# Performance work log

Measured on AMD Instinct MI355X. Metric: run time of the kernel, lower is better.

The kernel has to match this reference:

```python
import jax, jax.numpy as jnp
import numpy as np

B = 2048   # number of samples; acts as seq_len for the (S,N,E) transformer
DIN = 768
D = 512    # hidden_dim
H = 8      # nheads
HD = D // H
L = 3      # encoder layers
P = 40     # num_prototypes
Q = D // 4 # 128, projected feature dim
EPS = 1e-5


def setup_inputs() -> dict:
    key = jax.random.key(0)
    ks = jax.random.split(key, 22)
    s = 0.02
    rn = lambda k, shape: jax.random.normal(k, shape, jnp.float32) * s
    return {
        "x": jax.random.normal(ks[0], (B, DIN), jnp.float32),
        "reduce_w": rn(ks[1], (D, DIN)), "reduce_b": rn(ks[2], (D,)),
        "in_w": rn(ks[3], (L, 3 * D, D)), "in_b": rn(ks[4], (L, 3 * D)),
        "out_w": rn(ks[5], (L, D, D)), "out_b": rn(ks[6], (L, D)),
        "ff1_w": rn(ks[7], (L, D, D)), "ff1_b": rn(ks[8], (L, D)),
        "ff2_w": rn(ks[9], (L, D, D)), "ff2_b": rn(ks[10], (L, D)),
        "ln1_w": jnp.ones((L, D), jnp.float32), "ln1_b": jnp.zeros((L, D), jnp.float32),
        "ln2_w": jnp.ones((L, D), jnp.float32), "ln2_b": jnp.zeros((L, D), jnp.float32),
        "mlp_w1": rn(ks[11], (D, D)), "mlp_b1": rn(ks[12], (D,)),
        "mlp_w2": rn(ks[13], (D, D)), "mlp_b2": rn(ks[14], (D,)),
        "mlp_w3": rn(ks[15], (Q, D)), "mlp_b3": rn(ks[16], (Q,)),
        "highlights": jax.random.normal(ks[17], (P, Q), jnp.float32),
        "negatives": jax.random.normal(ks[18], (P, Q), jnp.float32),
    }


def _inorm(x):
    # InstanceNorm1d (affine=False) on a 2D tensor: per-row normalize over last dim
    m = x.mean(-1, keepdims=True)
    v = ((x - m) ** 2).mean(-1, keepdims=True)  # biased variance, matches torch
    return (x - m) * jax.lax.rsqrt(v + EPS)


def _ln(x, w, b):
    m = x.mean(-1, keepdims=True)
    v = ((x - m) ** 2).mean(-1, keepdims=True)
    return (x - m) * jax.lax.rsqrt(v + EPS) * w + b


def _cdist(a, cb):
    # euclidean distances [B,P]
    d2 = (a * a).sum(-1, keepdims=True) + (cb * cb).sum(-1) - 2.0 * a @ cb.T
    return jnp.sqrt(jnp.maximum(d2, 0.0))


def reference(x, reduce_w, reduce_b, in_w, in_b, out_w, out_b,
              ff1_w, ff1_b, ff2_w, ff2_b, ln1_w, ln1_b, ln2_w, ln2_b,
              mlp_w1, mlp_b1, mlp_w2, mlp_b2, mlp_w3, mlp_b3,
              highlights, negatives):
    feat0 = _inorm(x @ reduce_w.T + reduce_b)  # [B,D]

    # TransformerEncoder, post-norm, relu FFN, dropout off (eval).
    # Input is (seq=B, batch=1, D) -> attention across all B rows.
    feat = feat0
    scale = 1.0 / np.sqrt(HD)
    for i in range(L):
        qkv = feat @ in_w[i].T + in_b[i]           # [B,3D]
        q, k, v = jnp.split(qkv, 3, axis=-1)
        q = q.reshape(B, H, HD)
        k = k.reshape(B, H, HD)
        v = v.reshape(B, H, HD)
        scores = jnp.einsum('ihd,jhd->hij', q, k) * scale  # [H,B,B]
        attn = jax.nn.softmax(scores, axis=-1)
        ctx = jnp.einsum('hij,jhd->ihd', attn, v).reshape(B, D)
        attn_out = ctx @ out_w[i].T + out_b[i]
        feat = _ln(feat + attn_out, ln1_w[i], ln1_b[i])
        ff = jax.nn.relu(feat @ ff1_w[i].T + ff1_b[i]) @ ff2_w[i].T + ff2_b[i]
        feat = _ln(feat + ff, ln2_w[i], ln2_b[i])

    feat = feat0 + _inorm(feat)

    # MLP 512 -> 512 -> 512 -> 128 (relu on all but last)
    feat = jax.nn.relu(feat @ mlp_w1.T + mlp_b1)
    feat = jax.nn.relu(feat @ mlp_w2.T + mlp_b2)
    feat = feat @ mlp_w3.T + mlp_b3
    feat = _inorm(feat)  # [B,Q]

    positive_dist = _cdist(feat, highlights).min(-1)
    negative_dist = _cdist(feat, negatives).min(-1)
    logits = jnp.stack([-negative_dist, -positive_dist], axis=-1)  # [B,2]
    return logits
```

## Files before the change

kernel.cpp:

```cpp
#include <hip/hip_runtime.h>
#include <math.h>
#include <cstddef>

#define EPS 1e-5f

typedef __attribute__((ext_vector_type(8))) short bf16x8;
typedef __attribute__((ext_vector_type(4))) float f32x4;

__device__ __forceinline__ float wave_sum(float v) {
#pragma unroll
  for (int o = 32; o > 0; o >>= 1) v += __shfl_xor(v, o, 64);
  return v;
}

__device__ __forceinline__ unsigned short f2b(float f) {
  union { float f; unsigned int u; } v; v.f = f;
  unsigned int r = (v.u + 0x7FFFu + ((v.u >> 16) & 1u)) >> 16;
  return (unsigned short)r;
}
__device__ __forceinline__ float b2f(unsigned short u) {
  union { unsigned int u; float f; } v; v.u = ((unsigned int)u) << 16;
  return v.f;
}

__device__ __forceinline__ unsigned int pk2(float lo, float hi) {
  unsigned int r;
  asm volatile("v_cvt_pk_bf16_f32 %0, %1, %2" : "=v"(r) : "v"(lo), "v"(hi));
  return r;
}

struct WConvArgs {
  const float* src[8];
  unsigned short* dst[8];
  int n[8];
};
__global__ __launch_bounds__(256) void conv_w(WConvArgs a) {
  const int arr = blockIdx.y;
  const int i = (blockIdx.x * 256 + threadIdx.x) * 4;
  if (i >= a.n[arr]) return;
  const float4 f = *(const float4*)(a.src[arr] + i);
  unsigned short t[4] = {f2b(f.x), f2b(f.y), f2b(f.z), f2b(f.w)};
  unsigned short* d = a.dst[arr] + i;
  *(ushort2*)d = *(ushort2*)&t[0];
  *(ushort2*)(d + 2) = *(ushort2*)&t[2];
}

template <int RELU, int AF32, int OUT_F32, int OUT_BF16, int MERGE, int RESID,
          int SCALEQ>
__global__ __launch_bounds__(256) void gemm32(
    const void* __restrict__ Aptr, const float* __restrict__ pmp,
    const unsigned short* __restrict__ W, const float* __restrict__ bias,
    const float* __restrict__ Rf, float* __restrict__ Cf,
    unsigned short* __restrict__ Cb, int M, int N, int K) {
  __shared__ __align__(16) unsigned short As[2][32][72];
  __shared__ __align__(16) unsigned short Ws[2][64][72];
  const int tid = threadIdx.x;
  const int wid = tid >> 6, lane = tid & 63;
  const int ln = lane & 15, quad = lane >> 4;
  const int m0 = blockIdx.x * 32, n0 = blockIdx.y * 64;
  const int arow = tid >> 3, aseg = tid & 7;
  const int wrow = tid >> 2, wseg = tid & 3;
  const int KS = K >> 6;

  bf16x8 ra;
  float4 ra32[2];
  bf16x8 rwb0, rwb1;
  bf16x8 rp[4];
  float rl;

  auto load_tile = [&](int ks) {
    const int k0 = ks * 64;
    if (MERGE) {
      const int h = ks;
      const int row = m0 + arow;
      rl = 0.f;
#pragma unroll
      for (int s = 0; s < 4; ++s) {
        const size_t b = (size_t)((s * 8 + h) * 2048 + row);
        rl += pmp[b];
        rp[s] = *(const bf16x8*)((const unsigned short*)Aptr + b * 64 + aseg * 8);
      }
    } else if (AF32) {
      const float* ap = (const float*)Aptr + (size_t)(m0 + arow) * K + k0 + aseg * 8;
      ra32[0] = *(const float4*)ap;
      ra32[1] = *(const float4*)(ap + 4);
    } else {
      ra = *(const bf16x8*)((const unsigned short*)Aptr +
                            (size_t)(m0 + arow) * K + k0 + aseg * 8);
    }
    const unsigned short* wp = W + (size_t)(n0 + wrow) * K + k0 + wseg * 16;
    rwb0 = *(const bf16x8*)wp;
    rwb1 = *(const bf16x8*)(wp + 8);
  };

  auto store_tile = [&](int buf) {
    if (MERGE) {
      float inv = 1.f / rl;
      unsigned short ta[8];
#pragma unroll
      for (int j = 0; j < 8; ++j) {
        float s = b2f((unsigned short)rp[0][j]) + b2f((unsigned short)rp[1][j]) +
                  b2f((unsigned short)rp[2][j]) + b2f((unsigned short)rp[3][j]);
        ta[j] = f2b(inv * s);
      }
      *(bf16x8*)&As[buf][arow][aseg * 8] = *(const bf16x8*)&ta[0];
    } else if (AF32) {
      unsigned short ta[8];
      ta[0] = f2b(ra32[0].x); ta[1] = f2b(ra32[0].y);
      ta[2] = f2b(ra32[0].z); ta[3] = f2b(ra32[0].w);
      ta[4] = f2b(ra32[1].x); ta[5] = f2b(ra32[1].y);
      ta[6] = f2b(ra32[1].z); ta[7] = f2b(ra32[1].w);
      *(bf16x8*)&As[buf][arow][aseg * 8] = *(const bf16x8*)&ta[0];
    } else {
      *(bf16x8*)&As[buf][arow][aseg * 8] = ra;
    }
    *(bf16x8*)&Ws[buf][wrow][wseg * 16] = rwb0;
    *(bf16x8*)&Ws[buf][wrow][wseg * 16 + 8] = rwb1;
  };

  f32x4 acc[2];
  acc[0] = (f32x4){0.f, 0.f, 0.f, 0.f};
  acc[1] = (f32x4){0.f, 0.f, 0.f, 0.f};

  const int mrow = (wid & 1) * 16, nh = wid >> 1;

  load_tile(0);
  store_tile(0);
  __syncthreads();

#pragma unroll 1
  for (int ks = 0; ks < KS; ++ks) {
    const int cur = ks & 1;
    if (ks + 1 < KS) load_tile(ks + 1);
#pragma unroll
    for (int kc = 0; kc < 2; ++kc) {
      bf16x8 af = *(const bf16x8*)&As[cur][mrow + ln][kc * 32 + quad * 8];
#pragma unroll
      for (int nt = 0; nt < 2; ++nt) {
        bf16x8 wf = *(const bf16x8*)&Ws[cur][nh * 32 + nt * 16 + ln][kc * 32 + quad * 8];
        acc[nt] = __builtin_amdgcn_mfma_f32_16x16x32_bf16(af, wf, acc[nt], 0, 0, 0);
      }
    }
    if (ks + 1 < KS) store_tile(cur ^ 1);
    __syncthreads();
  }

  const int gm = m0 + mrow + quad * 4;
  const float qs = (SCALEQ && n0 < 512) ? 0.125f : 1.f;
#pragma unroll
  for (int nt = 0; nt < 2; ++nt) {
    const int gn = n0 + nh * 32 + nt * 16 + ln;
    float bv = bias[gn];
#pragma unroll
    for (int r = 0; r < 4; ++r) {
      float v = acc[nt][r] + bv;
      if (SCALEQ) v *= qs;
      if (RELU) v = fmaxf(v, 0.f);
      if (RESID) v += Rf[(size_t)(gm + r) * N + gn];
      if (OUT_F32) Cf[(size_t)(gm + r) * N + gn] = v;
      if (OUT_BF16) Cb[(size_t)(gm + r) * N + gn] = f2b(v);
    }
  }
}

__global__ __launch_bounds__(256) void flash_attn8(
    const unsigned short* __restrict__ qkv, float* __restrict__ pm,
    unsigned short* __restrict__ po) {
  __shared__ __align__(16) unsigned short Ks[64][72];
  __shared__ __align__(16) unsigned short Vt[64][72];
  __shared__ __align__(16) unsigned int Pp[64][36];
  const int qt = blockIdx.x, h = blockIdx.y, sp = blockIdx.z;
  const int tid = threadIdx.x;
  const int wid = tid >> 6, lane = tid & 63;
  const int ln = lane & 15, quad = lane >> 4;
  const int wq0 = wid * 16;

  bf16x8 aq[2];
  {
    const unsigned short* qp =
        qkv + (size_t)(qt * 64 + wq0 + ln) * 1536 + h * 64 + quad * 8;
    aq[0] = *(const bf16x8*)qp;
    aq[1] = *(const bf16x8*)(qp + 32);
  }

  const int key = tid >> 2, seg = tid & 3;
  bf16x8 rk0, rk1;
  unsigned short tv[16];

  auto load_kv = [&](int t) {
    const int g = sp * 8 + t;
    const unsigned short* kr =
        qkv + (size_t)(g * 64 + key) * 1536 + 512 + h * 64 + seg * 16;
    rk0 = *(const bf16x8*)kr;
    rk1 = *(const bf16x8*)(kr + 8);
#pragma unroll
    for (int j = 0; j < 16; ++j)
      tv[j] = qkv[(size_t)(g * 64 + wid * 16 + j) * 1536 + 1024 + h * 64 + lane];
  };
  auto store_kv = [&]() {
    *(bf16x8*)&Ks[key][seg * 16] = rk0;
    *(bf16x8*)&Ks[key][seg * 16 + 8] = rk1;
    *(bf16x8*)&Vt[lane][wid * 16] = *(const bf16x8*)&tv[0];
    *(bf16x8*)&Vt[lane][wid * 16 + 8] = *(const bf16x8*)&tv[8];
  };

  float l_r = 0.f;
  f32x4 acc_o[4];
#pragma unroll
  for (int nt = 0; nt < 4; ++nt) acc_o[nt] = (f32x4){0.f, 0.f, 0.f, 0.f};

  load_kv(0);
  store_kv();
  __syncthreads();

#pragma unroll 1
  for (int t = 0; t < 8; ++t) {
    if (t + 1 < 8) load_kv(t + 1);

    f32x4 s_acc[4];
#pragma unroll
    for (int nt = 0; nt < 4; ++nt) s_acc[nt] = (f32x4){0.f, 0.f, 0.f, 0.f};
#pragma unroll
    for (int nt = 0; nt < 4; ++nt) {
      bf16x8 kf0 = *(const bf16x8*)&Ks[nt * 16 + ln][quad * 8];
      bf16x8 kf1 = *(const bf16x8*)&Ks[nt * 16 + ln][32 + quad * 8];
      s_acc[nt] = __builtin_amdgcn_mfma_f32_16x16x32_bf16(kf0, aq[0], s_acc[nt], 0, 0, 0);
      s_acc[nt] = __builtin_amdgcn_mfma_f32_16x16x32_bf16(kf1, aq[1], s_acc[nt], 0, 0, 0);
    }

#pragma unroll
    for (int nt = 0; nt < 4; ++nt) {
      float p0 = __expf(s_acc[nt][0]);
      float p1 = __expf(s_acc[nt][1]);
      float p2 = __expf(s_acc[nt][2]);
      float p3 = __expf(s_acc[nt][3]);
      l_r += (p0 + p1) + (p2 + p3);
      uint2 w;
      w.x = pk2(p0, p1);
      w.y = pk2(p2, p3);
      *(uint2*)&Pp[wq0 + ln][nt * 8 + quad * 2] = w;
    }

#pragma unroll
    for (int kc = 0; kc < 2; ++kc) {
      bf16x8 pf = *(const bf16x8*)&Pp[wq0 + ln][kc * 16 + quad * 4];
#pragma unroll
      for (int nt = 0; nt < 4; ++nt) {
        bf16x8 vf = *(const bf16x8*)&Vt[nt * 16 + ln][kc * 32 + quad * 8];
        acc_o[nt] = __builtin_amdgcn_mfma_f32_16x16x32_bf16(pf, vf, acc_o[nt], 0, 0, 0);
      }
    }
    __syncthreads();
    if (t + 1 < 8) {
      store_kv();
      __syncthreads();
    }
  }

  const size_t base = (size_t)((sp * 8 + h) * 2048 + qt * 64);
  float l = l_r;
  l += __shfl_xor(l, 16, 64);
  l += __shfl_xor(l, 32, 64);
  if (quad == 0) pm[base + wq0 + ln] = l;
#pragma unroll
  for (int r = 0; r < 4; ++r) {
    const size_t row = base + wq0 + quad * 4 + r;
#pragma unroll
    for (int nt = 0; nt < 4; ++nt)
      po[row * 64 + nt * 16 + ln] = f2b(acc_o[nt][r]);
  }
}

__global__ __launch_bounds__(256) void inorm512(float* __restrict__ dst,
                                                unsigned short* __restrict__ dstb,
                                                const float* __restrict__ src) {
  const int row = blockIdx.x * 4 + (threadIdx.x >> 6);
  const int lane = threadIdx.x & 63;
  const float4* s = (const float4*)(src + (size_t)row * 512);
  float4 a = s[lane], b = s[lane + 64];
  float sum = a.x + a.y + a.z + a.w + b.x + b.y + b.z + b.w;
  float mean = wave_sum(sum) * (1.f / 512.f);
  float vs = (a.x - mean) * (a.x - mean) + (a.y - mean) * (a.y - mean) +
             (a.z - mean) * (a.z - mean) + (a.w - mean) * (a.w - mean) +
             (b.x - mean) * (b.x - mean) + (b.y - mean) * (b.y - mean) +
             (b.z - mean) * (b.z - mean) + (b.w - mean) * (b.w - mean);
  float rs = rsqrtf(wave_sum(vs) * (1.f / 512.f) + EPS);
  float4 oa, obv;
  oa.x = (a.x - mean) * rs; oa.y = (a.y - mean) * rs;
  oa.z = (a.z - mean) * rs; oa.w = (a.w - mean) * rs;
  obv.x = (b.x - mean) * rs; obv.y = (b.y - mean) * rs;
  obv.z = (b.z - mean) * rs; obv.w = (b.w - mean) * rs;
  float4* d = (float4*)(dst + (size_t)row * 512);
  d[lane] = oa; d[lane + 64] = obv;
  unsigned short* db = dstb + (size_t)row * 512;
  unsigned short t0[4] = {f2b(oa.x), f2b(oa.y), f2b(oa.z), f2b(oa.w)};
  unsigned short t1[4] = {f2b(obv.x), f2b(obv.y), f2b(obv.z), f2b(obv.w)};
  *(ushort2*)&db[lane * 4] = *(ushort2*)&t0[0];
  *(ushort2*)&db[lane * 4 + 2] = *(ushort2*)&t0[2];
  *(ushort2*)&db[256 + lane * 4] = *(ushort2*)&t1[0];
  *(ushort2*)&db[256 + lane * 4 + 2] = *(ushort2*)&t1[2];
}

__global__ __launch_bounds__(256) void ln_res2(float* __restrict__ dst,
                                               unsigned short* __restrict__ dstb,
                                               const float* __restrict__ src,
                                               const float* __restrict__ w,
                                               const float* __restrict__ bb) {
  const int row = blockIdx.x * 4 + (threadIdx.x >> 6);
  const int lane = threadIdx.x & 63;
  const float4* xs = (const float4*)(src + (size_t)row * 512);
  float4 a = xs[lane], b = xs[lane + 64];
  float sum = a.x + a.y + a.z + a.w + b.x + b.y + b.z + b.w;
  float mean = wave_sum(sum) * (1.f / 512.f);
  float vs = (a.x - mean) * (a.x - mean) + (a.y - mean) * (a.y - mean) +
             (a.z - mean) * (a.z - mean) + (a.w - mean) * (a.w - mean) +
             (b.x - mean) * (b.x - mean) + (b.y - mean) * (b.y - mean) +
             (b.z - mean) * (b.z - mean) + (b.w - mean) * (b.w - mean);
  float rs = rsqrtf(wave_sum(vs) * (1.f / 512.f) + EPS);
  float4 wa = ((const float4*)w)[lane], wb = ((const float4*)w)[lane + 64];
  float4 ba = ((const float4*)bb)[lane], bbv = ((const float4*)bb)[lane + 64];
  float4 oa, ob2;
  oa.x = (a.x - mean) * rs * wa.x + ba.x; oa.y = (a.y - mean) * rs * wa.y + ba.y;
  oa.z = (a.z - mean) * rs * wa.z + ba.z; oa.w = (a.w - mean) * rs * wa.w + ba.w;
  ob2.x = (b.x - mean) * rs * wb.x + bbv.x; ob2.y = (b.y - mean) * rs * wb.y + bbv.y;
  ob2.z = (b.z - mean) * rs * wb.z + bbv.z; ob2.w = (b.w - mean) * rs * wb.w + bbv.w;
  float4* d = (float4*)(dst + (size_t)row * 512);
  d[lane] = oa; d[lane + 64] = ob2;
  unsigned short* dbp = dstb + (size_t)row * 512;
  unsigned short t0[4] = {f2b(oa.x), f2b(oa.y), f2b(oa.z), f2b(oa.w)};
  unsigned short t1[4] = {f2b(ob2.x), f2b(ob2.y), f2b(ob2.z), f2b(ob2.w)};
  *(ushort2*)&dbp[lane * 4] = *(ushort2*)&t0[0];
  *(ushort2*)&dbp[lane * 4 + 2] = *(ushort2*)&t0[2];
  *(ushort2*)&dbp[256 + lane * 4] = *(ushort2*)&t1[0];
  *(ushort2*)&dbp[256 + lane * 4 + 2] = *(ushort2*)&t1[2];
}

__global__ __launch_bounds__(256) void add_inorm(float* __restrict__ feat,
                                                 unsigned short* __restrict__ featb,
                                                 const float* __restrict__ feat0) {
  const int row = blockIdx.x * 4 + (threadIdx.x >> 6);
  const int lane = threadIdx.x & 63;
  float4* f = (float4*)(feat + (size_t)row * 512);
  const float4* f0 = (const float4*)(feat0 + (size_t)row * 512);
  float4 a = f[lane], b = f[lane + 64];
  float sum = a.x + a.y + a.z + a.w + b.x + b.y + b.z + b.w;
  float mean = wave_sum(sum) * (1.f / 512.f);
  float vs = (a.x - mean) * (a.x - mean) + (a.y - mean) * (a.y - mean) +
             (a.z - mean) * (a.z - mean) + (a.w - mean) * (a.w - mean) +
             (b.x - mean) * (b.x - mean) + (b.y - mean) * (b.y - mean) +
             (b.z - mean) * (b.z - mean) + (b.w - mean) * (b.w - mean);
  float rs = rsqrtf(wave_sum(vs) * (1.f / 512.f) + EPS);
  float4 za = f0[lane], zb = f0[lane + 64];
  float4 oa, ob2;
  oa.x = za.x + (a.x - mean) * rs; oa.y = za.y + (a.y - mean) * rs;
  oa.z = za.z + (a.z - mean) * rs; oa.w = za.w + (a.w - mean) * rs;
  ob2.x = zb.x + (b.x - mean) * rs; ob2.y = zb.y + (b.y - mean) * rs;
  ob2.z = zb.z + (b.z - mean) * rs; ob2.w = zb.w + (b.w - mean) * rs;
  f[lane] = oa; f[lane + 64] = ob2;
  unsigned short* dbp = featb + (size_t)row * 512;
  unsigned short t0[4] = {f2b(oa.x), f2b(oa.y), f2b(oa.z), f2b(oa.w)};
  unsigned short t1[4] = {f2b(ob2.x), f2b(ob2.y), f2b(ob2.z), f2b(ob2.w)};
  *(ushort2*)&dbp[lane * 4] = *(ushort2*)&t0[0];
  *(ushort2*)&dbp[lane * 4 + 2] = *(ushort2*)&t0[2];
  *(ushort2*)&dbp[256 + lane * 4] = *(ushort2*)&t1[0];
  *(ushort2*)&dbp[256 + lane * 4 + 2] = *(ushort2*)&t1[2];
}

__global__ __launch_bounds__(256) void dist2(const float* __restrict__ fq,
                                             const float* __restrict__ hi,
                                             const float* __restrict__ ne,
                                             float* __restrict__ out) {
  const int row = blockIdx.x * 4 + (threadIdx.x >> 6);
  const int lane = threadIdx.x & 63;
  float f0 = fq[(size_t)row * 128 + lane];
  float f1 = fq[(size_t)row * 128 + 64 + lane];
  float mean = wave_sum(f0 + f1) * (1.f / 128.f);
  float vs = (f0 - mean) * (f0 - mean) + (f1 - mean) * (f1 - mean);
  float rs = rsqrtf(wave_sum(vs) * (1.f / 128.f) + EPS);
  f0 = (f0 - mean) * rs;
  f1 = (f1 - mean) * rs;
  float mp = 1e30f, mn = 1e30f;
  for (int p = 0; p < 40; ++p) {
    float h0 = hi[p * 128 + lane], h1 = hi[p * 128 + 64 + lane];
    float d0 = f0 - h0, d1 = f1 - h1;
    float d2 = wave_sum(d0 * d0 + d1 * d1);
    mp = fminf(mp, d2);
    float n0 = ne[p * 128 + lane], n1 = ne[p * 128 + 64 + lane];
    d0 = f0 - n0; d1 = f1 - n1;
    d2 = wave_sum(d0 * d0 + d1 * d1);
    mn = fminf(mn, d2);
  }
  if (lane == 0) {
    out[row * 2 + 0] = -sqrtf(mn);
    out[row * 2 + 1] = -sqrtf(mp);
  }
}

extern "C" void kernel_launch(void* const* d_in, const int* in_sizes, int n_in,
                              void* d_out, int out_size, void* d_ws, size_t ws_size,
                              hipStream_t stream) {
  const float* x        = (const float*)d_in[0];
  const float* reduce_w = (const float*)d_in[1];
  const float* reduce_b = (const float*)d_in[2];
  const float* in_w     = (const float*)d_in[3];
  const float* in_b     = (const float*)d_in[4];
  const float* out_w    = (const float*)d_in[5];
  const float* out_b    = (const float*)d_in[6];
  const float* ff1_w    = (const float*)d_in[7];
  const float* ff1_b    = (const float*)d_in[8];
  const float* ff2_w    = (const float*)d_in[9];
  const float* ff2_b    = (const float*)d_in[10];
  const float* ln1_w    = (const float*)d_in[11];
  const float* ln1_b    = (const float*)d_in[12];
  const float* ln2_w    = (const float*)d_in[13];
  const float* ln2_b    = (const float*)d_in[14];
  const float* mlp_w1   = (const float*)d_in[15];
  const float* mlp_b1   = (const float*)d_in[16];
  const float* mlp_w2   = (const float*)d_in[17];
  const float* mlp_b2   = (const float*)d_in[18];
  const float* mlp_w3   = (const float*)d_in[19];
  const float* mlp_b3   = (const float*)d_in[20];
  const float* hi       = (const float*)d_in[21];
  const float* ne       = (const float*)d_in[22];
  float* out = (float*)d_out;
  float* ws = (float*)d_ws;

  const size_t MD = (size_t)2048 * 512;
  float* feat0_f = ws;
  float* feat_f  = ws + MD;
  float* tmp_f   = ws + 2 * MD;
  float* pm      = ws + 3 * MD;
  unsigned short* u = (unsigned short*)(ws + 3 * MD + 65536);
  unsigned short* qkv_b   = u;
  unsigned short* feat0_b = u + 3 * MD;
  unsigned short* feat_b  = u + 4 * MD;
  unsigned short* relu_b  = u + 5 * MD;
  unsigned short* po_b    = u + 6 * MD;
  unsigned short* relu2_b = qkv_b;
  float* featq_f = tmp_f;

  unsigned short* wb = u + 10 * MD;
  unsigned short* reduce_wb = wb;
  unsigned short* in_wb     = wb + 393216;
  unsigned short* out_wb    = in_wb + 2359296;
  unsigned short* ff1_wb    = out_wb + 786432;
  unsigned short* ff2_wb    = ff1_wb + 786432;
  unsigned short* mlp_w1b   = ff2_wb + 786432;
  unsigned short* mlp_w2b   = mlp_w1b + 262144;
  unsigned short* mlp_w3b   = mlp_w2b + 262144;

  dim3 blk(256);
  WConvArgs wa;
  wa.src[0] = reduce_w; wa.dst[0] = reduce_wb; wa.n[0] = 393216;
  wa.src[1] = in_w;     wa.dst[1] = in_wb;     wa.n[1] = 2359296;
  wa.src[2] = out_w;    wa.dst[2] = out_wb;    wa.n[2] = 786432;
  wa.src[3] = ff1_w;    wa.dst[3] = ff1_wb;    wa.n[3] = 786432;
  wa.src[4] = ff2_w;    wa.dst[4] = ff2_wb;    wa.n[4] = 786432;
  wa.src[5] = mlp_w1;   wa.dst[5] = mlp_w1b;   wa.n[5] = 262144;
  wa.src[6] = mlp_w2;   wa.dst[6] = mlp_w2b;   wa.n[6] = 262144;
  wa.src[7] = mlp_w3;   wa.dst[7] = mlp_w3b;   wa.n[7] = 65536;
  conv_w<<<dim3(2304, 8), blk, 0, stream>>>(wa);

  gemm32<0, 1, 1, 0, 0, 0, 0><<<dim3(64, 8), blk, 0, stream>>>(
      x, nullptr, reduce_wb, reduce_b, nullptr, feat0_f, nullptr, 2048, 512, 768);
  inorm512<<<512, blk, 0, stream>>>(feat0_f, feat0_b, feat0_f);

  for (int i = 0; i < 3; ++i) {
    const float* fin_f = (i == 0) ? feat0_f : feat_f;
    const unsigned short* fin_b = (i == 0) ? feat0_b : feat_b;
    gemm32<0, 0, 0, 1, 0, 0, 1><<<dim3(64, 24), blk, 0, stream>>>(
        fin_b, nullptr, in_wb + (size_t)i * 1536 * 512, in_b + i * 1536,
        nullptr, nullptr, qkv_b, 2048, 1536, 512);
    flash_attn8<<<dim3(32, 8, 4), blk, 0, stream>>>(qkv_b, pm, po_b);
    gemm32<0, 0, 1, 0, 1, 1, 0><<<dim3(64, 8), blk, 0, stream>>>(
        po_b, pm, out_wb + (size_t)i * 512 * 512, out_b + i * 512,
        fin_f, tmp_f, nullptr, 2048, 512, 512);
    ln_res2<<<512, blk, 0, stream>>>(feat_f, feat_b, tmp_f,
                                     ln1_w + i * 512, ln1_b + i * 512);
    gemm32<1, 0, 0, 1, 0, 0, 0><<<dim3(64, 8), blk, 0, stream>>>(
        feat_b, nullptr, ff1_wb + (size_t)i * 512 * 512, ff1_b + i * 512,
        nullptr, nullptr, relu_b, 2048, 512, 512);
    gemm32<0, 0, 1, 0, 0, 1, 0><<<dim3(64, 8), blk, 0, stream>>>(
        relu_b, nullptr, ff2_wb + (size_t)i * 512 * 512, ff2_b + i * 512,
        feat_f, tmp_f, nullptr, 2048, 512, 512);
    ln_res2<<<512, blk, 0, stream>>>(feat_f, feat_b, tmp_f,
                                     ln2_w + i * 512, ln2_b + i * 512);
  }

  add_inorm<<<512, blk, 0, stream>>>(feat_f, feat_b, feat0_f);
  gemm32<1, 0, 0, 1, 0, 0, 0><<<dim3(64, 8), blk, 0, stream>>>(
      feat_b, nullptr, mlp_w1b, mlp_b1, nullptr, nullptr, relu_b, 2048, 512, 512);
  gemm32<1, 0, 0, 1, 0, 0, 0><<<dim3(64, 8), blk, 0, stream>>>(
      relu_b, nullptr, mlp_w2b, mlp_b2, nullptr, nullptr, relu2_b, 2048, 512, 512);
  gemm32<0, 0, 1, 0, 0, 0, 0><<<dim3(64, 2), blk, 0, stream>>>(
      relu2_b, nullptr, mlp_w3b, mlp_b3, nullptr, featq_f, nullptr, 2048, 128, 512);
  dist2<<<512, blk, 0, stream>>>(featq_f, hi, ne, out);
}
```

Before: 362.3 us.

## Replace LDS-tiled GEMM with register-resident, sync-free wave-tiled GEMM

Swaps the shared-memory double-buffered GEMM for a kernel where each wave keeps its whole A row-strip across K in registers and loads weight fragments straight from global memory, so there is no LDS staging and no barriers. Each wave now owns its own N-tile, grid shapes are retuned per call, and the attention-merge path normalises per head inside the register load. This removes LDS traffic and synchronisation, but uses more registers (A held for the full K) and relies on L2/cache for weight reuse across blocks, which may hurt occupancy or bandwidth.

```diff
diff --git a/kernel.cpp b/kernel.cpp
--- a/kernel.cpp
+++ b/kernel.cpp
@@ -27,6 +27,13 @@
   unsigned int r;
   asm volatile("v_cvt_pk_bf16_f32 %0, %1, %2" : "=v"(r) : "v"(lo), "v"(hi));
   return r;
+}
+
+__device__ __forceinline__ bf16x8 pack8(const float* o) {
+  union { unsigned int u[4]; bf16x8 v; } r;
+  r.u[0] = pk2(o[0], o[1]); r.u[1] = pk2(o[2], o[3]);
+  r.u[2] = pk2(o[4], o[5]); r.u[3] = pk2(o[6], o[7]);
+  return r.v;
 }
 
 struct WConvArgs {
@@ -45,120 +52,131 @@
   *(ushort2*)(d + 2) = *(ushort2*)&t[2];
 }
 
-template <int RELU, int AF32, int OUT_F32, int OUT_BF16, int MERGE, int RESID,
-          int SCALEQ>
-__global__ __launch_bounds__(256) void gemm32(
+template <int RELU, int APRO, int OUT_F32, int OUT_BF16, int RESID, int SCALEQ,
+          int MFRAGS, int NFRAGS, int KK>
+__global__ __launch_bounds__(256) void gemmw(
     const void* __restrict__ Aptr, const float* __restrict__ pmp,
     const unsigned short* __restrict__ W, const float* __restrict__ bias,
     const float* __restrict__ Rf, float* __restrict__ Cf,
-    unsigned short* __restrict__ Cb, int M, int N, int K) {
-  __shared__ __align__(16) unsigned short As[2][32][72];
-  __shared__ __align__(16) unsigned short Ws[2][64][72];
+    unsigned short* __restrict__ Cb, int N) {
   const int tid = threadIdx.x;
   const int wid = tid >> 6, lane = tid & 63;
   const int ln = lane & 15, quad = lane >> 4;
-  const int m0 = blockIdx.x * 32, n0 = blockIdx.y * 64;
-  const int arow = tid >> 3, aseg = tid & 7;
-  const int wrow = tid >> 2, wseg = tid & 3;
-  const int KS = K >> 6;
-
-  bf16x8 ra;
-  float4 ra32[2];
-  bf16x8 rwb0, rwb1;
-  bf16x8 rp[4];
-  float rl;
-
-  auto load_tile = [&](int ks) {
-    const int k0 = ks * 64;
-    if (MERGE) {
-      const int h = ks;
-      const int row = m0 + arow;
-      rl = 0.f;
-#pragma unroll
-      for (int s = 0; s < 4; ++s) {
-        const size_t b = (size_t)((s * 8 + h) * 2048 + row);
-        rl += pmp[b];
-        rp[s] = *(const bf16x8*)((const unsigned short*)Aptr + b * 64 + aseg * 8);
+  const int m0 = blockIdx.x * (16 * MFRAGS);
+  const int n0 = (blockIdx.y * 4 + wid) * (16 * NFRAGS);
+  constexpr int KC = KK / 32;
+
+  f32x4 acc[MFRAGS][NFRAGS];
+#pragma unroll
+  for (int mf = 0; mf < MFRAGS; ++mf)
+#pragma unroll
+    for (int nf = 0; nf < NFRAGS; ++nf)
+      acc[mf][nf] = (f32x4){0.f, 0.f, 0.f, 0.f};
+
+  const unsigned short* wp = W + (size_t)(n0 + ln) * KK + quad * 8;
+
+  if (APRO == 2) {
+    float linv[MFRAGS][8];
+#pragma unroll
+    for (int mf = 0; mf < MFRAGS; ++mf) {
+      const int row = m0 + mf * 16 + ln;
+#pragma unroll
+      for (int h = 0; h < 8; ++h)
+        linv[mf][h] = 1.f / (pmp[(size_t)h * 2048 + row] +
+                             pmp[(size_t)(8 + h) * 2048 + row] +
+                             pmp[(size_t)(16 + h) * 2048 + row] +
+                             pmp[(size_t)(24 + h) * 2048 + row]);
+    }
+    const unsigned short* pob = (const unsigned short*)Aptr;
+#pragma unroll
+    for (int kc = 0; kc < KC; ++kc) {
+      const int h = kc >> 1;
+      const int doff = (kc & 1) * 32 + quad * 8;
+      bf16x8 af[MFRAGS];
+#pragma unroll
+      for (int mf = 0; mf < MFRAGS; ++mf) {
+        const int row = m0 + mf * 16 + ln;
+        float o[8] = {0.f, 0.f, 0.f, 0.f, 0.f, 0.f, 0.f, 0.f};
+#pragma unroll
+        for (int s = 0; s < 4; ++s) {
+          bf16x8 v = *(const bf16x8*)(
+              pob + ((size_t)((s * 8 + h) * 2048 + row)) * 64 + doff);
+#pragma unroll
+          for (int k = 0; k < 8; ++k) o[k] += b2f((unsigned short)v[k]);
+        }
+        const float iv = linv[mf][h];
+#pragma unroll
+        for (int k = 0; k < 8; ++k) o[k] *= iv;
+        af[mf] = pack8(o);
       }
-    } else if (AF32) {
-      const float* ap = (const float*)Aptr + (size_t)(m0 + arow) * K + k0 + aseg * 8;
-      ra32[0] = *(const float4*)ap;
-      ra32[1] = *(const float4*)(ap + 4);
+      bf16x8 wf[NFRAGS];
+#pragma unroll
+      for (int nf = 0; nf < NFRAGS; ++nf)
+        wf[nf] = *(const bf16x8*)(wp + (size_t)nf * 16 * KK + kc * 32);
+#pragma unroll
+      for (int mf = 0; mf < MFRAGS; ++mf)
+#pragma unroll
+        for (int nf = 0; nf < NFRAGS; ++nf)
+          acc[mf][nf] = __builtin_amdgcn_mfma_f32_16x16x32_bf16(
+              af[mf], wf[nf], acc[mf][nf], 0, 0, 0);
+    }
+  } else {
+    bf16x8 areg[MFRAGS][KC];
+    if (APRO == 0) {
+#pragma unroll
+      for (int mf = 0; mf < MFRAGS; ++mf) {
+        const unsigned short* ap = (const unsigned short*)Aptr +
+                                   (size_t)(m0 + mf * 16 + ln) * KK + quad * 8;
+#pragma unroll
+        for (int kc = 0; kc < KC; ++kc)
+          areg[mf][kc] = *(const bf16x8*)(ap + kc * 32);
+      }
     } else {
-      ra = *(const bf16x8*)((const unsigned short*)Aptr +
-                            (size_t)(m0 + arow) * K + k0 + aseg * 8);
-    }
-    const unsigned short* wp = W + (size_t)(n0 + wrow) * K + k0 + wseg * 16;
-    rwb0 = *(const bf16x8*)wp;
-    rwb1 = *(const bf16x8*)(wp + 8);
-  };
-
-  auto store_tile = [&](int buf) {
-    if (MERGE) {
-      float inv = 1.f / rl;
-      unsigned short ta[8];
-#pragma unroll
-      for (int j = 0; j < 8; ++j) {
-        float s = b2f((unsigned short)rp[0][j]) + b2f((unsigned short)rp[1][j]) +
-                  b2f((unsigned short)rp[2][j]) + b2f((unsigned short)rp[3][j]);
-        ta[j] = f2b(inv * s);
+#pragma unroll
+      for (int mf = 0; mf < MFRAGS; ++mf) {
+        const float* ap =
+            (const float*)Aptr + (size_t)(m0 + mf * 16 + ln) * KK + quad * 8;
+#pragma unroll
+        for (int kc = 0; kc < KC; ++kc) {
+          float4 a = *(const float4*)(ap + kc * 32);
+          float4 b = *(const float4*)(ap + kc * 32 + 4);
+          float o[8] = {a.x, a.y, a.z, a.w, b.x, b.y, b.z, b.w};
+          areg[mf][kc] = pack8(o);
+        }
       }
-      *(bf16x8*)&As[buf][arow][aseg * 8] = *(const bf16x8*)&ta[0];
-    } else if (AF32) {
-      unsigned short ta[8];
-      ta[0] = f2b(ra32[0].x); ta[1] = f2b(ra32[0].y);
-      ta[2] = f2b(ra32[0].z); ta[3] = f2b(ra32[0].w);
-      ta[4] = f2b(ra32[1].x); ta[5] = f2b(ra32[1].y);
-      ta[6] = f2b(ra32[1].z); ta[7] = f2b(ra32[1].w);
-      *(bf16x8*)&As[buf][arow][aseg * 8] = *(const bf16x8*)&ta[0];
-    } else {
-      *(bf16x8*)&As[buf][arow][aseg * 8] = ra;
-    }
-    *(bf16x8*)&Ws[buf][wrow][wseg * 16] = rwb0;
-    *(bf16x8*)&Ws[buf][wrow][wseg * 16 + 8] = rwb1;
-  };
-
-  f32x4 acc[2];
-  acc[0] = (f32x4){0.f, 0.f, 0.f, 0.f};
-  acc[1] = (f32x4){0.f, 0.f, 0.f, 0.f};
-
-  const int mrow = (wid & 1) * 16, nh = wid >> 1;
-
-  load_tile(0);
-  store_tile(0);
-  __syncthreads();
-
-#pragma unroll 1
-  for (int ks = 0; ks < KS; ++ks) {
-    const int cur = ks & 1;
-    if (ks + 1 < KS) load_tile(ks + 1);
-#pragma unroll
-    for (int kc = 0; kc < 2; ++kc) {
-      bf16x8 af = *(const bf16x8*)&As[cur][mrow + ln][kc * 32 + quad * 8];
-#pragma unroll
-      for (int nt = 0; nt < 2; ++nt) {
-        bf16x8 wf = *(const bf16x8*)&Ws[cur][nh * 32 + nt * 16 + ln][kc * 32 + quad * 8];
-        acc[nt] = __builtin_amdgcn_mfma_f32_16x16x32_bf16(af, wf, acc[nt], 0, 0, 0);
+    }
+#pragma unroll
+    for (int kc = 0; kc < KC; ++kc) {
+      bf16x8 wf[NFRAGS];
+#pragma unroll
+      for (int nf = 0; nf < NFRAGS; ++nf)
+        wf[nf] = *(const bf16x8*)(wp + (size_t)nf * 16 * KK + kc * 32);
+#pragma unroll
+      for (int mf = 0; mf < MFRAGS; ++mf)
+#pragma unroll
+        for (int nf = 0; nf < NFRAGS; ++nf)
+          acc[mf][nf] = __builtin_amdgcn_mfma_f32_16x16x32_bf16(
+              areg[mf][kc], wf[nf], acc[mf][nf], 0, 0, 0);
+    }
+  }
+
+#pragma unroll
+  for (int mf = 0; mf < MFRAGS; ++mf) {
+    const int gm = m0 + mf * 16 + quad * 4;
+#pragma unroll
+    for (int nf = 0; nf < NFRAGS; ++nf) {
+      const int gn = n0 + nf * 16 + ln;
+      const float qs = (SCALEQ && (n0 + nf * 16) < 512) ? 0.125f : 1.f;
+      float bvv = bias[gn];
+#pragma unroll
+      for (int r = 0; r < 4; ++r) {
+        float v = acc[mf][nf][r] + bvv;
+        if (SCALEQ) v *= qs;
+        if (RELU) v = fmaxf(v, 0.f);
+        if (RESID) v += Rf[(size_t)(gm + r) * N + gn];
+        if (OUT_F32) Cf[(size_t)(gm + r) * N + gn] = v;
+        if (OUT_BF16) Cb[(size_t)(gm + r) * N + gn] = f2b(v);
       }
-    }
-    if (ks + 1 < KS) store_tile(cur ^ 1);
-    __syncthreads();
-  }
-
-  const int gm = m0 + mrow + quad * 4;
-  const float qs = (SCALEQ && n0 < 512) ? 0.125f : 1.f;
-#pragma unroll
-  for (int nt = 0; nt < 2; ++nt) {
-    const int gn = n0 + nh * 32 + nt * 16 + ln;
-    float bv = bias[gn];
-#pragma unroll
-    for (int r = 0; r < 4; ++r) {
-      float v = acc[nt][r] + bv;
-      if (SCALEQ) v *= qs;
-      if (RELU) v = fmaxf(v, 0.f);
-      if (RESID) v += Rf[(size_t)(gm + r) * N + gn];
-      if (OUT_F32) Cf[(size_t)(gm + r) * N + gn] = v;
-      if (OUT_BF16) Cb[(size_t)(gm + r) * N + gn] = f2b(v);
     }
   }
 }
@@ -461,38 +479,38 @@
   wa.src[7] = mlp_w3;   wa.dst[7] = mlp_w3b;   wa.n[7] = 65536;
   conv_w<<<dim3(2304, 8), blk, 0, stream>>>(wa);
 
-  gemm32<0, 1, 1, 0, 0, 0, 0><<<dim3(64, 8), blk, 0, stream>>>(
-      x, nullptr, reduce_wb, reduce_b, nullptr, feat0_f, nullptr, 2048, 512, 768);
+  gemmw<0, 1, 1, 0, 0, 0, 1, 2, 768><<<dim3(128, 4), blk, 0, stream>>>(
+      x, nullptr, reduce_wb, reduce_b, nullptr, feat0_f, nullptr, 512);
   inorm512<<<512, blk, 0, stream>>>(feat0_f, feat0_b, feat0_f);
 
   for (int i = 0; i < 3; ++i) {
     const float* fin_f = (i == 0) ? feat0_f : feat_f;
     const unsigned short* fin_b = (i == 0) ? feat0_b : feat_b;
-    gemm32<0, 0, 0, 1, 0, 0, 1><<<dim3(64, 24), blk, 0, stream>>>(
+    gemmw<0, 0, 0, 1, 0, 1, 2, 2, 512><<<dim3(64, 12), blk, 0, stream>>>(
         fin_b, nullptr, in_wb + (size_t)i * 1536 * 512, in_b + i * 1536,
-        nullptr, nullptr, qkv_b, 2048, 1536, 512);
+        nullptr, nullptr, qkv_b, 1536);
     flash_attn8<<<dim3(32, 8, 4), blk, 0, stream>>>(qkv_b, pm, po_b);
-    gemm32<0, 0, 1, 0, 1, 1, 0><<<dim3(64, 8), blk, 0, stream>>>(
+    gemmw<0, 2, 1, 0, 1, 0, 2, 4, 512><<<dim3(64, 2), blk, 0, stream>>>(
         po_b, pm, out_wb + (size_t)i * 512 * 512, out_b + i * 512,
-        fin_f, tmp_f, nullptr, 2048, 512, 512);
+        fin_f, tmp_f, nullptr, 512);
     ln_res2<<<512, blk, 0, stream>>>(feat_f, feat_b, tmp_f,
                                      ln1_w + i * 512, ln1_b + i * 512);
-    gemm32<1, 0, 0, 1, 0, 0, 0><<<dim3(64, 8), blk, 0, stream>>>(
+    gemmw<1, 0, 0, 1, 0, 0, 2, 2, 512><<<dim3(64, 4), blk, 0, stream>>>(
         feat_b, nullptr, ff1_wb + (size_t)i * 512 * 512, ff1_b + i * 512,
-        nullptr, nullptr, relu_b, 2048, 512, 512);
-    gemm32<0, 0, 1, 0, 0, 1, 0><<<dim3(64, 8), blk, 0, stream>>>(
+        nullptr, nullptr, relu_b, 512);
+    gemmw<0, 0, 1, 0, 1, 0, 2, 2, 512><<<dim3(64, 4), blk, 0, stream>>>(
         relu_b, nullptr, ff2_wb + (size_t)i * 512 * 512, ff2_b + i * 512,
-        feat_f, tmp_f, nullptr, 2048, 512, 512);
+        feat_f, tmp_f, nullptr, 512);
     ln_res2<<<512, blk, 0, stream>>>(feat_f, feat_b, tmp_f,
                                      ln2_w + i * 512, ln2_b + i * 512);
   }
 
   add_inorm<<<512, blk, 0, stream>>>(feat_f, feat_b, feat0_f);
-  gemm32<1, 0, 0, 1, 0, 0, 0><<<dim3(64, 8), blk, 0, stream>>>(
-      feat_b, nullptr, mlp_w1b, mlp_b1, nullptr, nullptr, relu_b, 2048, 512, 512);
-  gemm32<1, 0, 0, 1, 0, 0, 0><<<dim3(64, 8), blk, 0, stream>>>(
-      relu_b, nullptr, mlp_w2b, mlp_b2, nullptr, nullptr, relu2_b, 2048, 512, 512);
-  gemm32<0, 0, 1, 0, 0, 0, 0><<<dim3(64, 2), blk, 0, stream>>>(
-      relu2_b, nullptr, mlp_w3b, mlp_b3, nullptr, featq_f, nullptr, 2048, 128, 512);
+  gemmw<1, 0, 0, 1, 0, 0, 2, 2, 512><<<dim3(64, 4), blk, 0, stream>>>(
+      feat_b, nullptr, mlp_w1b, mlp_b1, nullptr, nullptr, relu_b, 512);
+  gemmw<1, 0, 0, 1, 0, 0, 2, 2, 512><<<dim3(64, 4), blk, 0, stream>>>(
+      relu_b, nullptr, mlp_w2b, mlp_b2, nullptr, nullptr, relu2_b, 512);
+  gemmw<0, 0, 1, 0, 0, 0, 2, 2, 512><<<dim3(64, 1), blk, 0, stream>>>(
+      relu2_b, nullptr, mlp_w3b, mlp_b3, nullptr, featq_f, nullptr, 128);
   dist2<<<512, blk, 0, stream>>>(featq_f, hi, ne, out);
 }
```

Result: slower. 560.0 us (+54.6%).
